# Kernel optimization log

Measured on AMD Instinct MI355X. Metric: run time of the kernel, lower is better.

Reference implementation:

```python
import jax, jax.numpy as jnp
import numpy as np

NUM_HEADS = 16


def _rope_tables(seq_len, head_dim, dtype):
    # angles[n, j] = n * 10000^(-2j/head_dim)
    pos = jnp.arange(seq_len, dtype=jnp.float32)
    inv = jnp.power(10000.0, -2.0 * jnp.arange(head_dim // 2, dtype=jnp.float32) / head_dim)
    ang = pos[:, None] * inv[None, :]                     # [N, D/2]
    # repeat_interleave(.., 2): [c0,c0,c1,c1,...]
    cos = jnp.repeat(jnp.cos(ang), 2, axis=-1).astype(dtype)  # [N, D]
    sin = jnp.repeat(jnp.sin(ang), 2, axis=-1).astype(dtype)  # [N, D]
    return cos[None, None], sin[None, None]               # [1,1,N,D]


def _rotate_half_interleaved(x):
    # stack([-x[...,1::2], x[...,::2]], -1).reshape_as(x)
    x2 = jnp.stack([-x[..., 1::2], x[..., ::2]], axis=-1)
    return x2.reshape(x.shape)


def setup_inputs() -> dict:
    key = jax.random.key(0)
    k0, k1, k2, k3 = jax.random.split(key, 4)
    B, N, C = 2, 2048, 1024
    s = 1.0 / np.sqrt(C)
    return {
        "x": jax.random.normal(k0, (B, N, C), dtype=jnp.float32),
        "Wq": jax.random.normal(k1, (C, C), dtype=jnp.float32) * s,
        "Wk": jax.random.normal(k2, (C, C), dtype=jnp.float32) * s,
        "Wv": jax.random.normal(k3, (C, C), dtype=jnp.float32) * s,
    }


def reference(x, Wq, Wk, Wv):
    B, N, C = x.shape
    H = NUM_HEADS
    D = C // H
    scale = D ** -0.5

    def heads(y):  # [B,N,C] -> [B,H,N,D]
        return y.reshape(B, N, H, D).transpose(0, 2, 1, 3)

    # nn.Linear: y = x @ W.T
    q = heads(x @ Wq.T)
    k = heads(x @ Wk.T)
    v = heads(x @ Wv.T)

    cos, sin = _rope_tables(N, D, x.dtype)
    q = q * cos + _rotate_half_interleaved(q) * sin
    k = k * cos + _rotate_half_interleaved(k) * sin

    attn = jnp.einsum("bhnd,bhmd->bhnm", q, k) * scale
    attn = jax.nn.softmax(attn, axis=-1)          # dropout p=0.0 -> identity
    out = jnp.einsum("bhnm,bhmd->bhnd", attn, v)
    return out.transpose(0, 2, 1, 3).reshape(B, N, C)
```

## Files before the change

kernel.cpp:

```cpp
#include <hip/hip_runtime.h>

typedef _Float16 f16;
typedef _Float16 f16x2 __attribute__((ext_vector_type(2)));
typedef _Float16 f16x8 __attribute__((ext_vector_type(8)));
typedef _Float16 f16x4 __attribute__((ext_vector_type(4)));
typedef float f32x4 __attribute__((ext_vector_type(4)));

#define GAS(p) ((const __attribute__((address_space(1))) void*)(p))
#define LAS(p) ((__attribute__((address_space(3))) void*)(p))

__device__ __forceinline__ f32x4 mfma16(f16x8 a, f16x8 b, f32x4 c) {
  return __builtin_amdgcn_mfma_f32_16x16x32_f16(a, b, c, 0, 0, 0);
}

__device__ __forceinline__ f16x2 cvt2(float a, float b) {
  return __builtin_bit_cast(f16x2, __builtin_amdgcn_cvt_pkrtz(a, b));
}

__device__ __forceinline__ void stage_tile(const f16* __restrict__ grow0,
                                           int stride_f16, f16* lds, int t) {
  int r = t >> 3;
  int sw = ((t & 7) ^ (r & 7)) * 8;
  __builtin_amdgcn_global_load_lds(GAS(grow0 + r * stride_f16 + sw),
                                   LAS(lds + t * 8), 16, 0, 0);
}

__global__ void convall(const float* __restrict__ x, const float* __restrict__ wq,
                        const float* __restrict__ wk, const float* __restrict__ wv,
                        f16* __restrict__ xh, f16* __restrict__ wh,
                        float* __restrict__ cosT, float* __restrict__ sinT) {
  int bid = blockIdx.x;
  if (bid >= 3584) {
    int idx = (bid - 3584) * 256 + threadIdx.x;
    int n = idx >> 5, jj = idx & 31;
    float inv = powf(10000.0f, -(float)jj * (1.0f / 32.0f));
    float ang = (float)n * inv;
    cosT[idx] = cosf(ang);
    sinT[idx] = sinf(ang);
    return;
  }
  const float* s;
  f16* d;
  int boff;
  if (bid < 2048)      { s = x;  d = xh;            boff = bid; }
  else if (bid < 2560) { s = wq; d = wh;            boff = bid - 2048; }
  else if (bid < 3072) { s = wk; d = wh + 1048576;  boff = bid - 2560; }
  else                 { s = wv; d = wh + 2097152;  boff = bid - 3072; }
  int i = (boff * 256 + threadIdx.x) * 8;
  float4 a = *(const float4*)(s + i);
  float4 b = *(const float4*)(s + i + 4);
  f16x8 o = {(f16)a.x, (f16)a.y, (f16)a.z, (f16)a.w,
             (f16)b.x, (f16)b.y, (f16)b.z, (f16)b.w};
  *(f16x8*)(d + i) = o;
}

__global__ __launch_bounds__(256, 3) void qkv_gemm(
    const f16* __restrict__ X, const f16* __restrict__ W,
    const float* __restrict__ cosT, const float* __restrict__ sinT,
    f16* __restrict__ Q, f16* __restrict__ K, f16* __restrict__ Vt) {
  __shared__ f16 As[128 * 64];
  __shared__ f16 Bs[128 * 64];
  const int tid = threadIdx.x;
  const int wv = tid >> 6, lane = tid & 63;
  const int m0 = blockIdx.x * 128, n0 = blockIdx.y * 128;
  const int cl = lane & 15, g = lane >> 4;
  const int wr = (wv >> 1) * 64, wc = (wv & 1) * 64;
  const int vx = cl & 7;

  f32x4 acc[4][4] = {};
  const f16* ga = X + (size_t)m0 * 1024;
  const f16* gb = W + (size_t)n0 * 1024;

  for (int kt = 0; kt < 1024; kt += 64) {
    __syncthreads();
#pragma unroll
    for (int rd = 0; rd < 4; ++rd) {
      stage_tile(ga + kt, 1024, As, tid + rd * 256);
      stage_tile(gb + kt, 1024, Bs, tid + rd * 256);
    }
    __syncthreads();
#pragma unroll
    for (int kk = 0; kk < 2; ++kk) {
      f16x8 a[4], bf[4];
#pragma unroll
      for (int mi = 0; mi < 4; ++mi)
        a[mi] = *(const f16x8*)(As + (wr + mi * 16 + cl) * 64 +
                                (((kk * 4 + g) ^ vx) << 3));
#pragma unroll
      for (int ni = 0; ni < 4; ++ni)
        bf[ni] = *(const f16x8*)(Bs + (wc + ni * 16 + cl) * 64 +
                                 (((kk * 4 + g) ^ vx) << 3));
#pragma unroll
      for (int mi = 0; mi < 4; ++mi)
#pragma unroll
        for (int ni = 0; ni < 4; ++ni)
          acc[mi][ni] = mfma16(a[mi], bf[ni], acc[mi][ni]);
    }
  }

  const int p = n0 >> 10;
  for (int mi = 0; mi < 4; ++mi) {
    int rbase = m0 + wr + mi * 16 + g * 4;
    for (int ni = 0; ni < 4; ++ni) {
      int gc = n0 + wc + ni * 16 + cl;
      int f = gc & 1023;
      int h = f >> 6, d = f & 63;
      if (p < 2) {
        int j = d >> 1;
        f16* dst = (p == 0) ? Q : K;
        float sc = (p == 0) ? 0.18033688011f : 1.0f;
        for (int r = 0; r < 4; ++r) {
          int row = rbase + r;
          int bb = row >> 11, n = row & 2047;
          float co = cosT[n * 32 + j], si = sinT[n * 32 + j];
          float v = acc[mi][ni][r];
          float pr = __shfl_xor(v, 1);
          float o = (d & 1) ? (v * co + pr * si) : (v * co - pr * si);
          dst[((bb * 16 + h) * 2048 + n) * 64 + d] = (f16)(o * sc);
        }
      } else {
        int bb = rbase >> 11, n = rbase & 2047;
        int np = (n & ~31) | (((n >> 2) & 3) << 3) | (((n >> 4) & 1) << 2);
        f16x4 pk = {(f16)acc[mi][ni][0], (f16)acc[mi][ni][1],
                    (f16)acc[mi][ni][2], (f16)acc[mi][ni][3]};
        *(f16x4*)(Vt + (size_t)((bb * 16 + h) * 64 + d) * 2048 + np) = pk;
      }
    }
  }
}

__global__ __launch_bounds__(128, 2) void attn(
    const f16* __restrict__ Q, const f16* __restrict__ K,
    const f16* __restrict__ Vt, float* __restrict__ out) {
  __shared__ f16 KB0[4096], VB0[4096], KB1[4096], VB1[4096];
  const int tid = threadIdx.x;
  const int w = tid >> 6, lane = tid & 63;
  const int cl = lane & 15, g = lane >> 4;
  const int id = blockIdx.x;
  const int xcd = id & 7, j = id >> 3;
  const int bh = xcd * 4 + (j >> 5);
  const int b = bh >> 4, h = bh & 15;
  const int qb = (j & 31) * 64 + w * 32;
  const f16* Qp = Q + (size_t)bh * (2048 * 64);
  const f16* Kp = K + (size_t)bh * (2048 * 64);
  const f16* Vp = Vt + (size_t)bh * (64 * 2048);

  f16x8 bq[2][2];
#pragma unroll
  for (int qh = 0; qh < 2; ++qh) {
    bq[qh][0] = *(const f16x8*)(Qp + (qb + qh * 16 + cl) * 64 + g * 8);
    bq[qh][1] = *(const f16x8*)(Qp + (qb + qh * 16 + cl) * 64 + 32 + g * 8);
  }

  f32x4 acc[2][4] = {};
  float lsp[2] = {0.f, 0.f};
  const int vx = cl & 7;
  const f32x4 z4 = {0.f, 0.f, 0.f, 0.f};

  auto STAGE = [&](int it, f16* kb, f16* vb) {
    const f16* kp = Kp + (size_t)it * 4096;
    const f16* vp = Vp + (size_t)it * 64;
#pragma unroll
    for (int rd = 0; rd < 4; ++rd) stage_tile(kp, 64, kb, tid + rd * 128);
#pragma unroll
    for (int rd = 0; rd < 4; ++rd) stage_tile(vp, 2048, vb, tid + rd * 128);
  };

  auto COMP = [&](const f16* kb, const f16* vb) {
    f16x8 a0[4], a1[4];
#pragma unroll
    for (int i = 0; i < 4; ++i) {
      const f16* kr = kb + (i * 16 + cl) * 64;
      a0[i] = *(const f16x8*)(kr + ((g ^ vx) << 3));
      a1[i] = *(const f16x8*)(kr + (((4 + g) ^ vx) << 3));
    }
    f32x4 s[2][4];
    __builtin_amdgcn_s_setprio(1);
#pragma unroll
    for (int qh = 0; qh < 2; ++qh)
#pragma unroll
      for (int i = 0; i < 4; ++i)
        s[qh][i] = mfma16(a1[i], bq[qh][1], mfma16(a0[i], bq[qh][0], z4));
    __builtin_amdgcn_s_setprio(0);
    union PB { f16x8 v; f16x2 hx[4]; };
    PB pbu[2][2];
#pragma unroll
    for (int qh = 0; qh < 2; ++qh) {
      float ps = 0.f;
#pragma unroll
      for (int i = 0; i < 4; ++i) {
        float p0 = exp2f(s[qh][i][0]);
        float p1 = exp2f(s[qh][i][1]);
        float p2 = exp2f(s[qh][i][2]);
        float p3 = exp2f(s[qh][i][3]);
        ps += (p0 + p1) + (p2 + p3);
        pbu[qh][i >> 1].hx[(i & 1) * 2] = cvt2(p0, p1);
        pbu[qh][i >> 1].hx[(i & 1) * 2 + 1] = cvt2(p2, p3);
      }
      lsp[qh] += ps;
    }
    __builtin_amdgcn_s_setprio(1);
#pragma unroll
    for (int ks = 0; ks < 2; ++ks) {
#pragma unroll
      for (int d = 0; d < 4; ++d) {
        const f16* vr = vb + (d * 16 + cl) * 64;
        f16x8 va = *(const f16x8*)(vr + (((ks * 4 + g) ^ vx) << 3));
        acc[0][d] = mfma16(va, pbu[0][ks].v, acc[0][d]);
        acc[1][d] = mfma16(va, pbu[1][ks].v, acc[1][d]);
      }
    }
    __builtin_amdgcn_s_setprio(0);
  };

  STAGE(0, KB0, VB0);
  STAGE(1, KB1, VB1);

  for (int t = 0; t < 15; ++t) {
    asm volatile("s_waitcnt vmcnt(8)" ::: "memory");
    __builtin_amdgcn_s_barrier();
    COMP(KB0, VB0);
    __builtin_amdgcn_s_barrier();
    STAGE(2 * t + 2, KB0, VB0);
    asm volatile("s_waitcnt vmcnt(8)" ::: "memory");
    __builtin_amdgcn_s_barrier();
    COMP(KB1, VB1);
    __builtin_amdgcn_s_barrier();
    STAGE(2 * t + 3, KB1, VB1);
  }
  asm volatile("s_waitcnt vmcnt(8)" ::: "memory");
  __builtin_amdgcn_s_barrier();
  COMP(KB0, VB0);
  asm volatile("s_waitcnt vmcnt(0)" ::: "memory");
  __builtin_amdgcn_s_barrier();
  COMP(KB1, VB1);

#pragma unroll
  for (int qh = 0; qh < 2; ++qh) {
    float ls = lsp[qh];
    ls += __shfl_xor(ls, 16);
    ls += __shfl_xor(ls, 32);
    float inv = 1.0f / ls;
    float* ob = out + (size_t)(b * 2048 + qb + qh * 16 + cl) * 1024 +
                h * 64 + g * 4;
#pragma unroll
    for (int d = 0; d < 4; ++d) {
      float4 o = {acc[qh][d][0] * inv, acc[qh][d][1] * inv,
                  acc[qh][d][2] * inv, acc[qh][d][3] * inv};
      *(float4*)(ob + (size_t)d * 16) = o;
    }
  }
}

extern "C" void kernel_launch(void* const* d_in, const int* in_sizes, int n_in,
                              void* d_out, int out_size, void* d_ws, size_t ws_size,
                              hipStream_t stream) {
  const float* x  = (const float*)d_in[0];
  const float* Wq = (const float*)d_in[1];
  const float* Wk = (const float*)d_in[2];
  const float* Wv = (const float*)d_in[3];
  float* out = (float*)d_out;
  char* ws = (char*)d_ws;

  f16* xh   = (f16*)(ws);
  f16* wh   = (f16*)(ws + 8388608);
  f16* Qr   = (f16*)(ws + 14680064);
  f16* Kr   = (f16*)(ws + 23068672);
  f16* Vt   = (f16*)(ws + 31457280);
  float* cosT = (float*)(ws + 39845888);
  float* sinT = (float*)(ws + 40108032);

  convall<<<3840, 256, 0, stream>>>(x, Wq, Wk, Wv, xh, wh, cosT, sinT);

  dim3 g1(32, 24);
  qkv_gemm<<<g1, 256, 0, stream>>>(xh, wh, cosT, sinT, Qr, Kr, Vt);

  attn<<<1024, 128, 0, stream>>>(Qr, Kr, Vt, out);
}
```

Before: 101.5 us.

## Split attention KV sequence across two wave pairs with LDS reduction

```diff
diff --git a/kernel.cpp b/kernel.cpp
--- a/kernel.cpp
+++ b/kernel.cpp
@@ -21,6 +21,14 @@
                                            int stride_f16, f16* lds, int t) {
   int r = t >> 3;
   int sw = ((t & 7) ^ (r & 7)) * 8;
+  __builtin_amdgcn_global_load_lds(GAS(grow0 + r * stride_f16 + sw),
+                                   LAS(lds + t * 8), 16, 0, 0);
+}
+
+__device__ __forceinline__ void stage_tile4(const f16* __restrict__ grow0,
+                                            int stride_f16, f16* lds, int t) {
+  int r = t >> 2;
+  int sw = ((t & 3) ^ (r & 3)) * 8;
   __builtin_amdgcn_global_load_lds(GAS(grow0 + r * stride_f16 + sw),
                                    LAS(lds + t * 8), 16, 0, 0);
 }
@@ -129,21 +137,25 @@
   }
 }
 
-__global__ __launch_bounds__(128, 2) void attn(
+__global__ __launch_bounds__(256, 4) void attn(
     const f16* __restrict__ Q, const f16* __restrict__ K,
     const f16* __restrict__ Vt, float* __restrict__ out) {
-  __shared__ f16 KB0[4096], VB0[4096], KB1[4096], VB1[4096];
+  __shared__ f16 SM[16384];
   const int tid = threadIdx.x;
   const int w = tid >> 6, lane = tid & 63;
   const int cl = lane & 15, g = lane >> 4;
+  const int s = w >> 1, wp = w & 1;
   const int id = blockIdx.x;
   const int xcd = id & 7, j = id >> 3;
   const int bh = xcd * 4 + (j >> 5);
   const int b = bh >> 4, h = bh & 15;
-  const int qb = (j & 31) * 64 + w * 32;
+  const int qb = (j & 31) * 64 + wp * 32;
   const f16* Qp = Q + (size_t)bh * (2048 * 64);
-  const f16* Kp = K + (size_t)bh * (2048 * 64);
-  const f16* Vp = Vt + (size_t)bh * (64 * 2048);
+  const f16* Kp = K + (size_t)bh * (2048 * 64) + (size_t)s * 65536;
+  const f16* Vp = Vt + (size_t)bh * (64 * 2048) + (size_t)s * 1024;
+
+  f16* Kb[2] = {SM + (s * 2 + 0) * 2048, SM + (s * 2 + 1) * 2048};
+  f16* Vb[2] = {SM + 8192 + (s * 2 + 0) * 2048, SM + 8192 + (s * 2 + 1) * 2048};
 
   f16x8 bq[2][2];
 #pragma unroll
@@ -154,100 +166,105 @@
 
   f32x4 acc[2][4] = {};
   float lsp[2] = {0.f, 0.f};
-  const int vx = cl & 7;
+  const int vx = cl & 7, vx3 = cl & 3;
   const f32x4 z4 = {0.f, 0.f, 0.f, 0.f};
-
-  auto STAGE = [&](int it, f16* kb, f16* vb) {
-    const f16* kp = Kp + (size_t)it * 4096;
-    const f16* vp = Vp + (size_t)it * 64;
-#pragma unroll
-    for (int rd = 0; rd < 4; ++rd) stage_tile(kp, 64, kb, tid + rd * 128);
-#pragma unroll
-    for (int rd = 0; rd < 4; ++rd) stage_tile(vp, 2048, vb, tid + rd * 128);
+  union PB { f16x8 v; f16x2 hx[4]; };
+
+  auto STAGE = [&](int it, int bf) {
+    if (wp == 0) {
+      const f16* kp = Kp + (size_t)it * 2048;
+#pragma unroll
+      for (int c = 0; c < 4; ++c) stage_tile(kp, 64, Kb[bf], lane + c * 64);
+    } else {
+      const f16* vp = Vp + (size_t)it * 32;
+#pragma unroll
+      for (int c = 0; c < 4; ++c) stage_tile4(vp, 2048, Vb[bf], lane + c * 64);
+    }
   };
 
-  auto COMP = [&](const f16* kb, const f16* vb) {
-    f16x8 a0[4], a1[4];
-#pragma unroll
-    for (int i = 0; i < 4; ++i) {
+  STAGE(0, 0);
+  for (int it = 0; it < 32; ++it) {
+    const int cur = it & 1;
+    asm volatile("s_waitcnt vmcnt(0)" ::: "memory");
+    __builtin_amdgcn_s_barrier();
+    if (it + 1 < 32) STAGE(it + 1, cur ^ 1);
+    const f16* kb = Kb[cur];
+    const f16* vb = Vb[cur];
+    f16x8 a0[2], a1[2];
+#pragma unroll
+    for (int i = 0; i < 2; ++i) {
       const f16* kr = kb + (i * 16 + cl) * 64;
       a0[i] = *(const f16x8*)(kr + ((g ^ vx) << 3));
       a1[i] = *(const f16x8*)(kr + (((4 + g) ^ vx) << 3));
     }
-    f32x4 s[2][4];
+    f32x4 sc[2][2];
     __builtin_amdgcn_s_setprio(1);
 #pragma unroll
     for (int qh = 0; qh < 2; ++qh)
 #pragma unroll
-      for (int i = 0; i < 4; ++i)
-        s[qh][i] = mfma16(a1[i], bq[qh][1], mfma16(a0[i], bq[qh][0], z4));
+      for (int i = 0; i < 2; ++i)
+        sc[qh][i] = mfma16(a1[i], bq[qh][1], mfma16(a0[i], bq[qh][0], z4));
     __builtin_amdgcn_s_setprio(0);
-    union PB { f16x8 v; f16x2 hx[4]; };
-    PB pbu[2][2];
+    PB pb[2];
 #pragma unroll
     for (int qh = 0; qh < 2; ++qh) {
-      float ps = 0.f;
-#pragma unroll
-      for (int i = 0; i < 4; ++i) {
-        float p0 = exp2f(s[qh][i][0]);
-        float p1 = exp2f(s[qh][i][1]);
-        float p2 = exp2f(s[qh][i][2]);
-        float p3 = exp2f(s[qh][i][3]);
-        ps += (p0 + p1) + (p2 + p3);
-        pbu[qh][i >> 1].hx[(i & 1) * 2] = cvt2(p0, p1);
-        pbu[qh][i >> 1].hx[(i & 1) * 2 + 1] = cvt2(p2, p3);
+      float p0 = exp2f(sc[qh][0][0]), p1 = exp2f(sc[qh][0][1]);
+      float p2 = exp2f(sc[qh][0][2]), p3 = exp2f(sc[qh][0][3]);
+      float p4 = exp2f(sc[qh][1][0]), p5 = exp2f(sc[qh][1][1]);
+      float p6 = exp2f(sc[qh][1][2]), p7 = exp2f(sc[qh][1][3]);
+      lsp[qh] += ((p0 + p1) + (p2 + p3)) + ((p4 + p5) + (p6 + p7));
+      pb[qh].hx[0] = cvt2(p0, p1); pb[qh].hx[1] = cvt2(p2, p3);
+      pb[qh].hx[2] = cvt2(p4, p5); pb[qh].hx[3] = cvt2(p6, p7);
+    }
+    __builtin_amdgcn_s_setprio(1);
+#pragma unroll
+    for (int d = 0; d < 4; ++d) {
+      const f16* vr = vb + (d * 16 + cl) * 32;
+      f16x8 va = *(const f16x8*)(vr + ((g ^ vx3) << 3));
+      acc[0][d] = mfma16(va, pb[0].v, acc[0][d]);
+      acc[1][d] = mfma16(va, pb[1].v, acc[1][d]);
+    }
+    __builtin_amdgcn_s_setprio(0);
+  }
+
+  float* CB = (float*)SM;
+  __syncthreads();
+  if (w >= 2) {
+    float* dst = CB + (size_t)wp * 2176 + lane * 34;
+#pragma unroll
+    for (int qh = 0; qh < 2; ++qh)
+#pragma unroll
+      for (int d = 0; d < 4; ++d)
+#pragma unroll
+        for (int r = 0; r < 4; ++r) dst[qh * 16 + d * 4 + r] = acc[qh][d][r];
+    dst[32] = lsp[0];
+    dst[33] = lsp[1];
+  }
+  __syncthreads();
+  if (w < 2) {
+    const float* src = CB + (size_t)wp * 2176 + lane * 34;
+#pragma unroll
+    for (int qh = 0; qh < 2; ++qh)
+#pragma unroll
+      for (int d = 0; d < 4; ++d)
+#pragma unroll
+        for (int r = 0; r < 4; ++r) acc[qh][d][r] += src[qh * 16 + d * 4 + r];
+    lsp[0] += src[32];
+    lsp[1] += src[33];
+#pragma unroll
+    for (int qh = 0; qh < 2; ++qh) {
+      float ls = lsp[qh];
+      ls += __shfl_xor(ls, 16);
+      ls += __shfl_xor(ls, 32);
+      float inv = 1.0f / ls;
+      float* ob = out + (size_t)(b * 2048 + qb + qh * 16 + cl) * 1024 +
+                  h * 64 + g * 4;
+#pragma unroll
+      for (int d = 0; d < 4; ++d) {
+        float4 o = {acc[qh][d][0] * inv, acc[qh][d][1] * inv,
+                    acc[qh][d][2] * inv, acc[qh][d][3] * inv};
+        *(float4*)(ob + (size_t)d * 16) = o;
       }
-      lsp[qh] += ps;
-    }
-    __builtin_amdgcn_s_setprio(1);
-#pragma unroll
-    for (int ks = 0; ks < 2; ++ks) {
-#pragma unroll
-      for (int d = 0; d < 4; ++d) {
-        const f16* vr = vb + (d * 16 + cl) * 64;
-        f16x8 va = *(const f16x8*)(vr + (((ks * 4 + g) ^ vx) << 3));
-        acc[0][d] = mfma16(va, pbu[0][ks].v, acc[0][d]);
-        acc[1][d] = mfma16(va, pbu[1][ks].v, acc[1][d]);
-      }
-    }
-    __builtin_amdgcn_s_setprio(0);
-  };
-
-  STAGE(0, KB0, VB0);
-  STAGE(1, KB1, VB1);
-
-  for (int t = 0; t < 15; ++t) {
-    asm volatile("s_waitcnt vmcnt(8)" ::: "memory");
-    __builtin_amdgcn_s_barrier();
-    COMP(KB0, VB0);
-    __builtin_amdgcn_s_barrier();
-    STAGE(2 * t + 2, KB0, VB0);
-    asm volatile("s_waitcnt vmcnt(8)" ::: "memory");
-    __builtin_amdgcn_s_barrier();
-    COMP(KB1, VB1);
-    __builtin_amdgcn_s_barrier();
-    STAGE(2 * t + 3, KB1, VB1);
-  }
-  asm volatile("s_waitcnt vmcnt(8)" ::: "memory");
-  __builtin_amdgcn_s_barrier();
-  COMP(KB0, VB0);
-  asm volatile("s_waitcnt vmcnt(0)" ::: "memory");
-  __builtin_amdgcn_s_barrier();
-  COMP(KB1, VB1);
-
-#pragma unroll
-  for (int qh = 0; qh < 2; ++qh) {
-    float ls = lsp[qh];
-    ls += __shfl_xor(ls, 16);
-    ls += __shfl_xor(ls, 32);
-    float inv = 1.0f / ls;
-    float* ob = out + (size_t)(b * 2048 + qb + qh * 16 + cl) * 1024 +
-                h * 64 + g * 4;
-#pragma unroll
-    for (int d = 0; d < 4; ++d) {
-      float4 o = {acc[qh][d][0] * inv, acc[qh][d][1] * inv,
-                  acc[qh][d][2] * inv, acc[qh][d][3] * inv};
-      *(float4*)(ob + (size_t)d * 16) = o;
     }
   }
 }
@@ -275,5 +292,5 @@
   dim3 g1(32, 24);
   qkv_gemm<<<g1, 256, 0, stream>>>(xh, wh, cosT, sinT, Qr, Kr, Vt);
 
-  attn<<<1024, 128, 0, stream>>>(Qr, Kr, Vt, out);
-}
+  attn<<<1024, 256, 0, stream>>>(Qr, Kr, Vt, out);
+}
```

After: 142.6 us. 40.6% more time.
